# Kernel optimization log

Hardware: AMD Instinct MI355X
Metric: run time of the kernel (lower is better)

## Reference

```python
import jax, jax.numpy as jnp
import numpy as np

N = 8192
F_IN = 512
F_OUT = 256
NEG_SLOPE = 0.01  # F.leaky_relu default
MASK_VAL = -1000000000000000.0


def setup_inputs() -> dict:
    key = jax.random.key(0)
    k1, k2, k3, k4 = jax.random.split(key, 4)
    stdv = 1.0 / np.sqrt(F_OUT)
    x = jax.random.normal(k1, (N, F_IN), dtype=jnp.float32)
    weight = jax.random.uniform(k2, (F_IN, F_OUT), dtype=jnp.float32, minval=-stdv, maxval=stdv)
    att_vec = jax.random.normal(k3, (2 * F_OUT, 1), dtype=jnp.float32) * 0.05
    adj = jax.random.randint(k4, (N, N), 0, 2, dtype=jnp.int32)
    return {"x": x, "weight": weight, "att_vec": att_vec, "adj": adj}


def _pair_indices(n):
    # Reproduces the (buggy-but-faithful) torch.cat(dim=0).view(n,-1,2f) indexing:
    # element (i,j,:f)  = out[idx(2m)], element (i,j,f:) = out[idx(2m+1)], m = i*n+j
    # idx(r) = r // n if r < n*n else (r - n*n) % n
    nn_ = n * n
    m = jnp.arange(nn_, dtype=jnp.int32)
    r0 = 2 * m
    r1 = r0 + 1
    idx1 = jnp.where(r0 < nn_, r0 // n, (r0 - nn_) % n)
    idx2 = jnp.where(r1 < nn_, r1 // n, (r1 - nn_) % n)
    return idx1, idx2


def reference(x, weight, att_vec, adj):
    n = x.shape[0]
    f = weight.shape[1]
    # dropout p=0.0 -> identity
    out = x @ weight                      # (n, f)
    a1 = att_vec[:f, 0]                   # (f,)
    a2 = att_vec[f:, 0]                   # (f,)
    s1 = out @ a1                         # (n,)
    s2 = out @ a2                         # (n,)
    idx1, idx2 = _pair_indices(n)
    scores = (s1[idx1] + s2[idx2]).reshape(n, n)
    scores = jax.nn.leaky_relu(scores, NEG_SLOPE)
    scores = jnp.where(adj > 0, scores, MASK_VAL)
    attn = jax.nn.softmax(scores, axis=1)  # F.softmax default dim=1 for 2D
    return jax.nn.sigmoid(attn @ out)      # (n, f)
```

## Files before the change

### kernel.cpp

```cpp
#include <hip/hip_runtime.h>

using u32 = unsigned int;
using u16 = unsigned short;

typedef __attribute__((ext_vector_type(8)))  __bf16 bf16x8;
typedef __attribute__((ext_vector_type(16))) float  f32x16;
typedef __attribute__((ext_vector_type(4)))  float  f32x4;
typedef __attribute__((ext_vector_type(4)))  int    i32x4;

__device__ __forceinline__ u32 f2bf(float f){
  u32 u = __float_as_uint(f);
  return (u + 0x7FFFu + ((u >> 16) & 1u)) >> 16;
}
__device__ __forceinline__ u32 pack2bf(float lo, float hi){
  return f2bf(lo) | (f2bf(hi) << 16);
}
__device__ __forceinline__ float bfu2f(u32 us){ return __uint_as_float(us << 16); }
__device__ __forceinline__ float lrelu(float x){ return x > 0.f ? x : 0.01f * x; }

__global__ void k0_wt(const float* __restrict__ w, u16* __restrict__ wT){
  int u = blockIdx.x * 256 + threadIdx.x;
  int k = u >> 8, n = u & 255;
  wT[(size_t)n * 512 + k] = (u16)f2bf(w[(size_t)k * 256 + n]);
}

__global__ __launch_bounds__(512, 2) void k1_gemm(const float* __restrict__ x,
    const u16* __restrict__ wT, const float* __restrict__ av, u16* __restrict__ outF,
    float* __restrict__ v0, float* __restrict__ v1, u16* __restrict__ pbf){
  __shared__ float tb[8][32][36];
  __shared__ float afl[512];
  __shared__ float sred[2][32][17];
  __shared__ float srw[2][32];
  const int i0 = blockIdx.x * 32;
  const int tid = threadIdx.x;
  const int lane = tid & 63, wv = tid >> 6;
  const int r = lane & 31, h = lane >> 5;
  const float* xp = x + (size_t)(i0 + r) * 512 + h * 8;
  const u16*   bp = wT + (size_t)(wv * 32 + r) * 512 + h * 8;
  f32x16 acc = {};
  for (int s = 0; s < 32; ++s){
    f32x4 a0 = *(const f32x4*)xp;
    f32x4 a1 = *(const f32x4*)(xp + 4);
    i32x4 pk = { (int)pack2bf(a0[0], a0[1]), (int)pack2bf(a0[2], a0[3]),
                 (int)pack2bf(a1[0], a1[1]), (int)pack2bf(a1[2], a1[3]) };
    bf16x8 af = __builtin_bit_cast(bf16x8, pk);
    bf16x8 bf = *(const bf16x8*)bp;
    acc = __builtin_amdgcn_mfma_f32_32x32x16_bf16(af, bf, acc, 0, 0, 0);
    xp += 16; bp += 16;
  }
  #pragma unroll
  for (int re = 0; re < 16; ++re){
    int rr = (re & 3) + 8 * (re >> 2) + 4 * h;
    tb[wv][r][rr] = acc[re];
  }
  afl[tid] = av[tid];
  __syncthreads();
  {
    const int n2 = lane >> 1, ic = (lane & 1) * 16;
    const float* tp = &tb[wv][n2][ic];
    i32x4 w0 = { (int)pack2bf(tp[0],tp[1]),   (int)pack2bf(tp[2],tp[3]),
                 (int)pack2bf(tp[4],tp[5]),   (int)pack2bf(tp[6],tp[7]) };
    i32x4 w1 = { (int)pack2bf(tp[8],tp[9]),   (int)pack2bf(tp[10],tp[11]),
                 (int)pack2bf(tp[12],tp[13]), (int)pack2bf(tp[14],tp[15]) };
    const int n = wv * 32 + n2;
    const int k16 = (i0 + ic) >> 4;
    u16* op = outF + ((size_t)k16 * 256 + n) * 16;
    *(i32x4*)op = w0;
    *((i32x4*)op + 1) = w1;
  }
  const int row = tid & 31, g = tid >> 5;
  const int w8 = g >> 1, fh = (g & 1) * 16;
  float a1c = 0.f, a2c = 0.f;
  #pragma unroll
  for (int f = 0; f < 16; ++f){
    float tv = tb[w8][fh + f][row];
    a1c = fmaf(tv, afl[w8 * 32 + fh + f], a1c);
    a2c = fmaf(tv, afl[256 + w8 * 32 + fh + f], a2c);
  }
  sred[0][row][g] = a1c; sred[1][row][g] = a2c;
  __syncthreads();
  if (tid < 64){
    int which = tid >> 5, r2 = tid & 31;
    float s = 0.f;
    #pragma unroll
    for (int g2 = 0; g2 < 16; ++g2) s += sred[which][r2][g2];
    srw[which][r2] = s;
  }
  __syncthreads();
  if (tid < 16){
    int k = (i0 >> 1) + tid;
    float sa  = srw[0][2*tid],   sb  = srw[1][2*tid];
    float sa1 = srw[0][2*tid+1], sb1 = srw[1][2*tid+1];
    v0[k] = lrelu(sa + sb);
    v1[k] = lrelu(sa1 + sb1);
    float w = lrelu(sa + sb1);
    pbf[k] = (u16)f2bf(__expf(w));
  }
}

__global__ __launch_bounds__(512, 2) void k3_main(const int* __restrict__ adj,
    const u16* __restrict__ outF, const u16* __restrict__ pbf,
    float* __restrict__ P, float* __restrict__ pd){
  __shared__ u16 AbS[2][16768];
  __shared__ u32 plS[1024];
  __shared__ float dshS[64];
  const int bid = blockIdx.x;
  const int xcd = bid & 7, slot = bid >> 3;
  const int half = xcd & 1, c = xcd >> 1;
  const int tile = half * 64 + slot;
  const bool top = half == 0;
  const int i0 = tile * 64;
  const int kbase = c * 2048;
  const int pb = tile * 4 + c;
  const int tid = threadIdx.x, l = tid & 63, w = tid >> 6;
  const int r = l & 31, h = l >> 5, fb = w * 32;
  const int* aq0 = adj + (size_t)(i0 + w) * 8192 + kbase + l * 4;
  const u16* bq0 = outF + (size_t)c * 524288 + (fb + r) * 16 + h * 8;
  const int sl_ = l >> 2, hp_ = (l >> 1) & 1, off_ = 4 * (l & 1);
  u16* const wp0 = &AbS[0][0] + sl_ * 1048 + hp_ * 512 + off_;
  const u16* const rp0 = &AbS[0][0] + h * 512 + r * 8;

  if (top){
    plS[tid] = 0x3F803F80u; plS[tid + 512] = 0x3F803F80u;
  } else {
    const u32* ps = (const u32*)pbf + (c & 1) * 1024;
    plS[tid] = ps[tid]; plS[tid + 512] = ps[tid + 512];
  }
  __syncthreads();

  i32x4 arA[4], arB[4];
  bf16x8 BA[4], BB[4];
  f32x16 acc0 = {}, acc1 = {};
  float dA[4] = {0.f,0.f,0.f,0.f}, dB[4] = {0.f,0.f,0.f,0.f};

#define ADJ_SET(AR_,Q0_,T_) { \
  _Pragma("unroll") for (int q_ = 0; q_ < 4; ++q_) \
    AR_[q_] = *(const i32x4*)(aq0 + (size_t)((Q0_) + q_) * 65536 + (T_) * 256); \
  asm volatile("" ::: "memory"); }

#define B_ISS4(B_,G_) { const u16* bb_ = bq0 + (size_t)(G_) * 4096; \
  B_[0] = *(const bf16x8*)bb_;          B_[1] = *(const bf16x8*)(bb_ + 4096); \
  B_[2] = *(const bf16x8*)(bb_ + 8192); B_[3] = *(const bf16x8*)(bb_ + 12288); \
  asm volatile("" ::: "memory"); }

#define MFMA4(B_,BUF_,S0_) { \
  const u16* rb_ = rp0 + (BUF_) * 16768 + (S0_) * 1048; \
  __builtin_amdgcn_s_setprio(1); \
  _Pragma("unroll") for (int j_ = 0; j_ < 4; ++j_){ \
    bf16x8 a0_ = *(const bf16x8*)(rb_ + j_ * 1048); \
    bf16x8 a1_ = *(const bf16x8*)(rb_ + j_ * 1048 + 256); \
    acc0 = __builtin_amdgcn_mfma_f32_32x32x16_bf16(a0_, B_[j_], acc0, 0, 0, 0); \
    acc1 = __builtin_amdgcn_mfma_f32_32x32x16_bf16(a1_, B_[j_], acc1, 0, 0, 0); } \
  __builtin_amdgcn_s_setprio(0); }

#define PACK_SET(AR_,D_,RB_,T_,BUF_) { \
  _Pragma("unroll") for (int q_ = 0; q_ < 4; ++q_){ \
    const int row_ = (RB_) * 32 + q_ * 8 + w; \
    i32x4 a_ = AR_[q_]; \
    u32 p0_ = plS[((T_) & 7) * 128 + 2 * l]; \
    u32 p1_ = plS[((T_) & 7) * 128 + 2 * l + 1]; \
    u32 w0_ = ((((u32)(-a_[0])) & 0xFFFFu) | (((u32)(-a_[1])) << 16)) & p0_; \
    u32 w1_ = ((((u32)(-a_[2])) & 0xFFFFu) | (((u32)(-a_[3])) << 16)) & p1_; \
    D_[q_] += __uint_as_float(w0_ << 16) + __uint_as_float(w0_ & 0xFFFF0000u) \
            + __uint_as_float(w1_ << 16) + __uint_as_float(w1_ & 0xFFFF0000u); \
    uint2 wv_; wv_.x = w0_; wv_.y = w1_; \
    *(uint2*)(wp0 + (BUF_) * 16768 + row_ * 8) = wv_; } }

#define KBAR() { asm volatile("s_waitcnt lgkmcnt(0)" ::: "memory"); \
  __builtin_amdgcn_s_barrier(); asm volatile("" ::: "memory"); }

  ADJ_SET(arA, 0, 0);
  ADJ_SET(arB, 4, 0);
  B_ISS4(BA, 0);
  PACK_SET(arA, dA, 0, 0, 0);
  PACK_SET(arB, dB, 1, 0, 0);
  KBAR();

  #pragma unroll 1
  for (int t = 0; t < 8; ++t){
    const int buf = t & 1;
    const int g0 = t * 16;
    B_ISS4(BB, g0 + 4);
    if (t < 7) ADJ_SET(arA, 0, t + 1);
    MFMA4(BA, buf, 0);
    B_ISS4(BA, g0 + 8);
    if (t < 7) ADJ_SET(arB, 4, t + 1);
    MFMA4(BB, buf, 4);
    B_ISS4(BB, g0 + 12);
    MFMA4(BA, buf, 8);
    if (t < 7){ B_ISS4(BA, g0 + 16); }
    MFMA4(BB, buf, 12);
    if (t < 7){
      PACK_SET(arA, dA, 0, t + 1, buf ^ 1);
      PACK_SET(arB, dB, 1, t + 1, buf ^ 1);
      KBAR();
    }
  }

#undef ADJ_SET
#undef B_ISS4
#undef MFMA4
#undef PACK_SET
#undef KBAR

  #pragma unroll
  for (int q = 0; q < 4; ++q){
    float vA = dA[q], vB = dB[q];
    #pragma unroll
    for (int mk = 1; mk < 64; mk <<= 1){
      vA += __shfl_xor(vA, mk);
      vB += __shfl_xor(vB, mk);
    }
    if (l == 0){ dshS[q * 8 + w] = vA; dshS[32 + q * 8 + w] = vB; }
  }
  __syncthreads();
  if (tid < 64) pd[(size_t)pb * 64 + tid] = dshS[tid];
  float* Pb = P + (size_t)pb * 16384 + fb + r;
  #pragma unroll
  for (int e = 0; e < 16; ++e){
    int rr = (e & 3) + 8 * (e >> 2) + 4 * h;
    __builtin_nontemporal_store(acc0[e], Pb + (size_t)rr * 256);
    __builtin_nontemporal_store(acc1[e], Pb + (size_t)(rr + 32) * 256);
  }
}

__global__ void k4_final(const float* __restrict__ P, const float* __restrict__ pd,
    const float* __restrict__ v0, const float* __restrict__ v1, float* __restrict__ out){
  const int i = blockIdx.x, n = threadIdx.x;
  const int tile = i >> 6, rloc = i & 63;
  const size_t base = ((size_t)tile * 4 * 64 + rloc) * 256 + n;
  float P0 = __builtin_nontemporal_load(P + base);
  float P1 = __builtin_nontemporal_load(P + base + 16384);
  float P2 = __builtin_nontemporal_load(P + base + 32768);
  float P3 = __builtin_nontemporal_load(P + base + 49152);
  const float* pdp = pd + (size_t)tile * 256 + rloc;
  float d0 = pdp[0], d1 = pdp[64], d2 = pdp[128], d3 = pdp[192];
  float val;
  if (i < 4096){
    float va = v0[i], vb = v1[i];
    float m = fmaxf(va, vb);
    float e0 = __expf(va - m), e1 = __expf(vb - m);
    val = (e0 * (P0 + P1 + P2 + P3) * 0.f + e0 * (P0 + P1 + P2 + P3)) /
          (1.f);
    val = (e0 * (P0 + P1) + e1 * (P2 + P3)) / (e0 * (d0 + d1) + e1 * (d2 + d3));
  } else {
    val = (P0 + P1 + P2 + P3) / (d0 + d1 + d2 + d3);
  }
  out[(size_t)i * 256 + n] = 1.0f / (1.0f + __expf(-val));
}

extern "C" void kernel_launch(void* const* d_in, const int* in_sizes, int n_in,
                              void* d_out, int out_size, void* d_ws, size_t ws_size,
                              hipStream_t stream)
{
  const float* x      = (const float*)d_in[0];
  const float* weight = (const float*)d_in[1];
  const float* av     = (const float*)d_in[2];
  const int*   adj    = (const int*)d_in[3];
  float* out = (float*)d_out;
  char* ws = (char*)d_ws;
  float* P     = (float*)(ws + 0);
  float* pd    = (float*)(ws + 33554432);
  u16*   outF  = (u16*)  (ws + 33685504);
  u16*   wT    = (u16*)  (ws + 37879808);
  u16*   pbf   = (u16*)  (ws + 38141952);
  float* v0    = (float*)(ws + 38150144);
  float* v1    = (float*)(ws + 38166528);

  k0_wt    <<<512, 256, 0, stream>>>(weight, wT);
  k1_gemm  <<<256, 512, 0, stream>>>(x, wT, av, outF, v0, v1, pbf);
  k3_main  <<<512, 512, 0, stream>>>(adj, outF, pbf, P, pd);
  k4_final <<<8192, 256, 0, stream>>>(P, pd, v0, v1, out);
}
```

Baseline: 111.2 us.

## Pre-pack adjacency into bitmask and retile main kernel to 4 waves

Adds a kernel that compresses the int32 adjacency matrix into a 1-bit-per-entry mask. The main attention kernel then reads this mask instead of the raw int32 values, which cuts its global load traffic and register pressure. The main kernel also drops from 8 to 4 waves per block, with each wave computing four 32x32 accumulators instead of two. The full adjacency read still happens once in the new pack kernel, which adds a launch and a mask round-trip through memory. The per-row denominator reduction now writes directly from each wave instead of going through shared memory.

```diff
diff --git a/kernel.cpp b/kernel.cpp
--- a/kernel.cpp
+++ b/kernel.cpp
@@ -98,12 +98,32 @@
   }
 }
 
-__global__ __launch_bounds__(512, 2) void k3_main(const int* __restrict__ adj,
+__global__ __launch_bounds__(256, 2) void k2bm(const int* __restrict__ adj,
+                                               u32* __restrict__ bm){
+  const int row = blockIdx.x * 4 + (threadIdx.x >> 6);
+  const int l = threadIdx.x & 63;
+  const int* ap = adj + (size_t)row * 8192 + l * 32;
+  u32* bp = bm + (size_t)row * 256 + l;
+  #pragma unroll
+  for (int it = 0; it < 4; ++it){
+    i32x4 v[8];
+    #pragma unroll
+    for (int j = 0; j < 8; ++j) v[j] = *(const i32x4*)(ap + it * 2048 + j * 4);
+    u32 m = 0;
+    #pragma unroll
+    for (int j = 0; j < 8; ++j){
+      m |= ((u32)v[j][0] << (4*j))   | ((u32)v[j][1] << (4*j+1))
+         | ((u32)v[j][2] << (4*j+2)) | ((u32)v[j][3] << (4*j+3));
+    }
+    bp[it * 64] = m;
+  }
+}
+
+__global__ __launch_bounds__(256, 2) void k3_main(const u32* __restrict__ bm,
     const u16* __restrict__ outF, const u16* __restrict__ pbf,
     float* __restrict__ P, float* __restrict__ pd){
   __shared__ u16 AbS[2][16768];
   __shared__ u32 plS[1024];
-  __shared__ float dshS[64];
   const int bid = blockIdx.x;
   const int xcd = bid & 7, slot = bid >> 3;
   const int half = xcd & 1, c = xcd >> 1;
@@ -112,35 +132,37 @@
   const int i0 = tile * 64;
   const int kbase = c * 2048;
   const int pb = tile * 4 + c;
-  const int tid = threadIdx.x, l = tid & 63, w = tid >> 6;
-  const int r = l & 31, h = l >> 5, fb = w * 32;
-  const int* aq0 = adj + (size_t)(i0 + w) * 8192 + kbase + l * 4;
-  const u16* bq0 = outF + (size_t)c * 524288 + (fb + r) * 16 + h * 8;
-  const int sl_ = l >> 2, hp_ = (l >> 1) & 1, off_ = 4 * (l & 1);
-  u16* const wp0 = &AbS[0][0] + sl_ * 1048 + hp_ * 512 + off_;
+  const int tid = threadIdx.x, l = tid & 63, w4 = tid >> 6;
+  const int r = l & 31, h = l >> 5;
+  const u16* bq0 = outF + (size_t)c * 524288 + (w4 * 64 + r) * 16 + h * 8;
+  const u32* bmq = bm + (size_t)(i0 + w4) * 256 + (kbase >> 5) + (l >> 3);
+  u16* const wp0 = &AbS[0][0] + (l >> 2) * 1048 + ((l >> 1) & 1) * 512 + 4 * (l & 1);
   const u16* const rp0 = &AbS[0][0] + h * 512 + r * 8;
+  const int sh4 = 4 * (l & 7);
 
   if (top){
-    plS[tid] = 0x3F803F80u; plS[tid + 512] = 0x3F803F80u;
+    plS[tid] = 0x3F803F80u; plS[tid + 256] = 0x3F803F80u;
+    plS[tid + 512] = 0x3F803F80u; plS[tid + 768] = 0x3F803F80u;
   } else {
     const u32* ps = (const u32*)pbf + (c & 1) * 1024;
-    plS[tid] = ps[tid]; plS[tid + 512] = ps[tid + 512];
-  }
-  __syncthreads();
-
-  i32x4 arA[4], arB[4];
-  bf16x8 BA[4], BB[4];
-  f32x16 acc0 = {}, acc1 = {};
-  float dA[4] = {0.f,0.f,0.f,0.f}, dB[4] = {0.f,0.f,0.f,0.f};
-
-#define ADJ_SET(AR_,Q0_,T_) { \
-  _Pragma("unroll") for (int q_ = 0; q_ < 4; ++q_) \
-    AR_[q_] = *(const i32x4*)(aq0 + (size_t)((Q0_) + q_) * 65536 + (T_) * 256); \
+    plS[tid] = ps[tid]; plS[tid + 256] = ps[tid + 256];
+    plS[tid + 512] = ps[tid + 512]; plS[tid + 768] = ps[tid + 768];
+  }
+  __syncthreads();
+
+  u32 bmr[16];
+  bf16x8 BA[8], BB[8];
+  f32x16 a00 = {}, a01 = {}, a10 = {}, a11 = {};
+  float dd[16] = {0.f,0.f,0.f,0.f,0.f,0.f,0.f,0.f,0.f,0.f,0.f,0.f,0.f,0.f,0.f,0.f};
+
+#define BM_LOAD(T_) { _Pragma("unroll") for (int q_ = 0; q_ < 16; ++q_) \
+    bmr[q_] = bmq[(size_t)q_ * 1024 + (T_) * 8]; \
   asm volatile("" ::: "memory"); }
 
-#define B_ISS4(B_,G_) { const u16* bb_ = bq0 + (size_t)(G_) * 4096; \
-  B_[0] = *(const bf16x8*)bb_;          B_[1] = *(const bf16x8*)(bb_ + 4096); \
-  B_[2] = *(const bf16x8*)(bb_ + 8192); B_[3] = *(const bf16x8*)(bb_ + 12288); \
+#define B_ISS(B_,G_) { const u16* bb_ = bq0 + (size_t)(G_) * 4096; \
+  _Pragma("unroll") for (int j_ = 0; j_ < 4; ++j_){ \
+    B_[2*j_]   = *(const bf16x8*)(bb_ + j_ * 4096); \
+    B_[2*j_+1] = *(const bf16x8*)(bb_ + j_ * 4096 + 512); } \
   asm volatile("" ::: "memory"); }
 
 #define MFMA4(B_,BUF_,S0_) { \
@@ -149,78 +171,73 @@
   _Pragma("unroll") for (int j_ = 0; j_ < 4; ++j_){ \
     bf16x8 a0_ = *(const bf16x8*)(rb_ + j_ * 1048); \
     bf16x8 a1_ = *(const bf16x8*)(rb_ + j_ * 1048 + 256); \
-    acc0 = __builtin_amdgcn_mfma_f32_32x32x16_bf16(a0_, B_[j_], acc0, 0, 0, 0); \
-    acc1 = __builtin_amdgcn_mfma_f32_32x32x16_bf16(a1_, B_[j_], acc1, 0, 0, 0); } \
+    a00 = __builtin_amdgcn_mfma_f32_32x32x16_bf16(a0_, B_[2*j_],   a00, 0, 0, 0); \
+    a01 = __builtin_amdgcn_mfma_f32_32x32x16_bf16(a0_, B_[2*j_+1], a01, 0, 0, 0); \
+    a10 = __builtin_amdgcn_mfma_f32_32x32x16_bf16(a1_, B_[2*j_],   a10, 0, 0, 0); \
+    a11 = __builtin_amdgcn_mfma_f32_32x32x16_bf16(a1_, B_[2*j_+1], a11, 0, 0, 0); } \
   __builtin_amdgcn_s_setprio(0); }
 
-#define PACK_SET(AR_,D_,RB_,T_,BUF_) { \
-  _Pragma("unroll") for (int q_ = 0; q_ < 4; ++q_){ \
-    const int row_ = (RB_) * 32 + q_ * 8 + w; \
-    i32x4 a_ = AR_[q_]; \
-    u32 p0_ = plS[((T_) & 7) * 128 + 2 * l]; \
-    u32 p1_ = plS[((T_) & 7) * 128 + 2 * l + 1]; \
-    u32 w0_ = ((((u32)(-a_[0])) & 0xFFFFu) | (((u32)(-a_[1])) << 16)) & p0_; \
-    u32 w1_ = ((((u32)(-a_[2])) & 0xFFFFu) | (((u32)(-a_[3])) << 16)) & p1_; \
-    D_[q_] += __uint_as_float(w0_ << 16) + __uint_as_float(w0_ & 0xFFFF0000u) \
+#define PACK(T_,BUF_) { \
+  u32 p0_ = plS[(T_) * 128 + 2 * l]; \
+  u32 p1_ = plS[(T_) * 128 + 2 * l + 1]; \
+  _Pragma("unroll") for (int q_ = 0; q_ < 16; ++q_){ \
+    u32 e_ = (bmr[q_] >> sh4) & 0xFu; \
+    u32 w0_ = (((u32)-(int)(e_ & 1u)) & 0xFFFFu) | (((u32)-(int)((e_>>1)&1u)) & 0xFFFF0000u); \
+    u32 w1_ = (((u32)-(int)((e_>>2)&1u)) & 0xFFFFu) | (((u32)-(int)((e_>>3)&1u)) & 0xFFFF0000u); \
+    w0_ &= p0_; w1_ &= p1_; \
+    dd[q_] += __uint_as_float(w0_ << 16) + __uint_as_float(w0_ & 0xFFFF0000u) \
             + __uint_as_float(w1_ << 16) + __uint_as_float(w1_ & 0xFFFF0000u); \
     uint2 wv_; wv_.x = w0_; wv_.y = w1_; \
-    *(uint2*)(wp0 + (BUF_) * 16768 + row_ * 8) = wv_; } }
+    *(uint2*)(wp0 + (BUF_) * 16768 + (q_ * 4 + w4) * 8) = wv_; } }
 
 #define KBAR() { asm volatile("s_waitcnt lgkmcnt(0)" ::: "memory"); \
   __builtin_amdgcn_s_barrier(); asm volatile("" ::: "memory"); }
 
-  ADJ_SET(arA, 0, 0);
-  ADJ_SET(arB, 4, 0);
-  B_ISS4(BA, 0);
-  PACK_SET(arA, dA, 0, 0, 0);
-  PACK_SET(arB, dB, 1, 0, 0);
+  BM_LOAD(0);
+  B_ISS(BA, 0);
+  PACK(0, 0);
   KBAR();
 
   #pragma unroll 1
   for (int t = 0; t < 8; ++t){
     const int buf = t & 1;
     const int g0 = t * 16;
-    B_ISS4(BB, g0 + 4);
-    if (t < 7) ADJ_SET(arA, 0, t + 1);
+    B_ISS(BB, g0 + 4);
+    if (t < 7) BM_LOAD(t + 1);
     MFMA4(BA, buf, 0);
-    B_ISS4(BA, g0 + 8);
-    if (t < 7) ADJ_SET(arB, 4, t + 1);
+    B_ISS(BA, g0 + 8);
     MFMA4(BB, buf, 4);
-    B_ISS4(BB, g0 + 12);
+    B_ISS(BB, g0 + 12);
     MFMA4(BA, buf, 8);
-    if (t < 7){ B_ISS4(BA, g0 + 16); }
+    if (t < 7){ B_ISS(BA, g0 + 16); }
     MFMA4(BB, buf, 12);
     if (t < 7){
-      PACK_SET(arA, dA, 0, t + 1, buf ^ 1);
-      PACK_SET(arB, dB, 1, t + 1, buf ^ 1);
+      PACK(t + 1, buf ^ 1);
       KBAR();
     }
   }
 
-#undef ADJ_SET
-#undef B_ISS4
+#undef BM_LOAD
+#undef B_ISS
 #undef MFMA4
-#undef PACK_SET
+#undef PACK
 #undef KBAR
 
   #pragma unroll
-  for (int q = 0; q < 4; ++q){
-    float vA = dA[q], vB = dB[q];
-    #pragma unroll
-    for (int mk = 1; mk < 64; mk <<= 1){
-      vA += __shfl_xor(vA, mk);
-      vB += __shfl_xor(vB, mk);
-    }
-    if (l == 0){ dshS[q * 8 + w] = vA; dshS[32 + q * 8 + w] = vB; }
-  }
-  __syncthreads();
-  if (tid < 64) pd[(size_t)pb * 64 + tid] = dshS[tid];
-  float* Pb = P + (size_t)pb * 16384 + fb + r;
+  for (int q = 0; q < 16; ++q){
+    float v = dd[q];
+    #pragma unroll
+    for (int mk = 1; mk < 64; mk <<= 1) v += __shfl_xor(v, mk);
+    if (l == 0) pd[(size_t)pb * 64 + q * 4 + w4] = v;
+  }
+  float* Pb = P + (size_t)pb * 16384 + w4 * 64 + r;
   #pragma unroll
   for (int e = 0; e < 16; ++e){
     int rr = (e & 3) + 8 * (e >> 2) + 4 * h;
-    __builtin_nontemporal_store(acc0[e], Pb + (size_t)rr * 256);
-    __builtin_nontemporal_store(acc1[e], Pb + (size_t)(rr + 32) * 256);
+    __builtin_nontemporal_store(a00[e], Pb + (size_t)rr * 256);
+    __builtin_nontemporal_store(a01[e], Pb + (size_t)rr * 256 + 32);
+    __builtin_nontemporal_store(a10[e], Pb + (size_t)(rr + 32) * 256);
+    __builtin_nontemporal_store(a11[e], Pb + (size_t)(rr + 32) * 256 + 32);
   }
 }
 
@@ -240,8 +257,6 @@
     float va = v0[i], vb = v1[i];
     float m = fmaxf(va, vb);
     float e0 = __expf(va - m), e1 = __expf(vb - m);
-    val = (e0 * (P0 + P1 + P2 + P3) * 0.f + e0 * (P0 + P1 + P2 + P3)) /
-          (1.f);
     val = (e0 * (P0 + P1) + e1 * (P2 + P3)) / (e0 * (d0 + d1) + e1 * (d2 + d3));
   } else {
     val = (P0 + P1 + P2 + P3) / (d0 + d1 + d2 + d3);
@@ -266,9 +281,11 @@
   u16*   pbf   = (u16*)  (ws + 38141952);
   float* v0    = (float*)(ws + 38150144);
   float* v1    = (float*)(ws + 38166528);
-
-  k0_wt    <<<512, 256, 0, stream>>>(weight, wT);
-  k1_gemm  <<<256, 512, 0, stream>>>(x, wT, av, outF, v0, v1, pbf);
-  k3_main  <<<512, 512, 0, stream>>>(adj, outF, pbf, P, pd);
-  k4_final <<<8192, 256, 0, stream>>>(P, pd, v0, v1, out);
-}
+  u32*   bm    = (u32*)  (ws + 38182912);
+
+  k0_wt   <<<512, 256, 0, stream>>>(weight, wT);
+  k2bm    <<<2048, 256, 0, stream>>>(adj, bm);
+  k1_gemm <<<256, 512, 0, stream>>>(x, wT, av, outF, v0, v1, pbf);
+  k3_main <<<512, 256, 0, stream>>>(bm, outF, pbf, P, pd);
+  k4_final<<<8192, 256, 0, stream>>>(P, pd, v0, v1, out);
+}
```

Measured after the change: 137.9 us. +24.0%, slower.
